# Kernel tuning notes

Measured on AMD Instinct MI355X. Metric: run time of the kernel, lower is better.

The kernel has to match this reference:

```python
import jax, jax.numpy as jnp
import numpy as np

N = 100000
EPS_BN = 1e-5


def setup_inputs() -> dict:
    key = jax.random.key(0)
    ks = jax.random.split(key, 12)
    x = jax.random.normal(ks[0], (N, 128), dtype=jnp.float32)
    edge_index = jax.random.randint(ks[1], (2, 800000), 0, N, dtype=jnp.int64)
    # GCNConv layer params (PyG: lin weight [out,in], bias added after aggregation)
    s = 1.0 / np.sqrt(128.0)
    W1 = jax.random.uniform(ks[2], (128, 128), jnp.float32, -s, s)
    b1 = jnp.zeros((128,), jnp.float32)
    W2 = jax.random.uniform(ks[3], (128, 128), jnp.float32, -s, s)
    b2 = jnp.zeros((128,), jnp.float32)
    # BatchNorm affine params
    g1 = jnp.ones((128,), jnp.float32)
    be1 = jnp.zeros((128,), jnp.float32)
    g2 = jnp.ones((128,), jnp.float32)
    be2 = jnp.zeros((128,), jnp.float32)
    # PReLU single shared parameter (torch init = 0.25)
    a = jnp.asarray(0.25, jnp.float32)
    return {"x": x, "edge_index": edge_index, "W1": W1, "b1": b1, "g1": g1,
            "be1": be1, "W2": W2, "b2": b2, "g2": g2, "be2": be2, "a": a}


def _gcn_conv(x, src, dst, deg_inv_sqrt, W, b):
    # x' = D^-1/2 (A+I) D^-1/2 (x W^T) + b  (self loops already in src/dst)
    h = x @ W.T                                   # [N, out]
    norm = deg_inv_sqrt[src] * deg_inv_sqrt[dst]  # [E+N]
    msg = h[src] * norm[:, None]                  # gather + scale
    out = jax.ops.segment_sum(msg, dst, num_segments=N)  # scatter-add
    return out + b


def _batchnorm(x, g, be):
    # training-mode BatchNorm1d over nodes (biased variance)
    mean = jnp.mean(x, axis=0)
    var = jnp.mean(jnp.square(x - mean), axis=0)
    return (x - mean) * jax.lax.rsqrt(var + EPS_BN) * g + be


def _prelu(x, a):
    return jnp.where(x > 0, x, a * x)


def reference(x, edge_index, W1, b1, g1, be1, W2, b2, g2, be2, a):
    # add self loops
    loops = jnp.arange(N, dtype=edge_index.dtype)
    src = jnp.concatenate([edge_index[0], loops])
    dst = jnp.concatenate([edge_index[1], loops])
    # symmetric normalization from in-degree at destinations
    deg = jax.ops.segment_sum(jnp.ones_like(dst, dtype=x.dtype), dst, num_segments=N)
    deg_inv_sqrt = jnp.where(deg > 0, jax.lax.rsqrt(deg), 0.0)

    h = _gcn_conv(x, src, dst, deg_inv_sqrt, W1, b1)
    h = _prelu(_batchnorm(h, g1, be1), a)
    h = _gcn_conv(h, src, dst, deg_inv_sqrt, W2, b2)
    h = _prelu(_batchnorm(h, g2, be2), a)
    return h
```

## Files before the change

### kernel.cpp

```cpp
#include <hip/hip_runtime.h>
#include <cstddef>
#include <cstdint>


#define EPS_BN 1e-5f
#define BN_BLOCKS 256

typedef short short8 __attribute__((ext_vector_type(8)));
typedef float f32x4 __attribute__((ext_vector_type(4)));

static __device__ __forceinline__ unsigned short f2b(float f) {
    union { float f; uint32_t u; } v; v.f = f;
    uint32_t u = v.u;
    return (unsigned short)((u + 0x7FFFu + ((u >> 16) & 1u)) >> 16);
}
static __device__ __forceinline__ float b2f(unsigned short h) {
    union { uint32_t u; float f; } v; v.u = ((uint32_t)h) << 16;
    return v.f;
}
static __device__ __forceinline__ float b2f_s(short h) { return b2f((unsigned short)h); }

__global__ __launch_bounds__(256) void k_count(const int* __restrict__ dst, int* __restrict__ cnt, int E) {
    int e = blockIdx.x * 256 + threadIdx.x;
    if (e < E) atomicAdd(&cnt[dst[e]], 1);
}

__global__ __launch_bounds__(256) void k_scanA(const int* __restrict__ cnt, int* __restrict__ partial, int n) {
    __shared__ int sd[256];
    int tid = threadIdx.x;
    int base = blockIdx.x * 1024 + tid * 4;
    int s = 0;
#pragma unroll
    for (int j = 0; j < 4; j++) { int idx = base + j; if (idx < n) s += cnt[idx]; }
    sd[tid] = s; __syncthreads();
    for (int off = 128; off > 0; off >>= 1) {
        if (tid < off) sd[tid] += sd[tid + off];
        __syncthreads();
    }
    if (tid == 0) partial[blockIdx.x] = sd[0];
}

__global__ __launch_bounds__(128) void k_scanB(int* partial, int nb) {
    __shared__ int sd[128];
    int t = threadIdx.x;
    sd[t] = (t < nb) ? partial[t] : 0;
    __syncthreads();
    for (int off = 1; off < 128; off <<= 1) {
        int v = (t >= off) ? sd[t - off] : 0;
        __syncthreads();
        sd[t] += v;
        __syncthreads();
    }
    if (t < nb) partial[t] = (t == 0) ? 0 : sd[t - 1];
}

__global__ __launch_bounds__(256) void k_scanC(const int* __restrict__ cnt, const int* __restrict__ partial,
                                               int* __restrict__ rowptr, float* __restrict__ dis, int n) {
    __shared__ int sd[256];
    int tid = threadIdx.x;
    int base = blockIdx.x * 1024 + tid * 4;
    int v[4]; int s = 0;
#pragma unroll
    for (int j = 0; j < 4; j++) { int idx = base + j; v[j] = (idx < n) ? cnt[idx] : 0; s += v[j]; }
    sd[tid] = s; __syncthreads();
    for (int off = 1; off < 256; off <<= 1) {
        int u = (tid >= off) ? sd[tid - off] : 0;
        __syncthreads();
        sd[tid] += u;
        __syncthreads();
    }
    int excl = partial[blockIdx.x] + ((tid == 0) ? 0 : sd[tid - 1]);
#pragma unroll
    for (int j = 0; j < 4; j++) {
        int idx = base + j;
        if (idx < n) {
            rowptr[idx] = excl;
            dis[idx] = rsqrtf((float)(v[j] + 1));
        }
        excl += v[j];
    }
}

__global__ __launch_bounds__(256) void k_fill(const int* __restrict__ src, const int* __restrict__ dst,
                                              const int* __restrict__ rowptr, int* __restrict__ fillc,
                                              int* __restrict__ colw, int E) {
    int e = blockIdx.x * 256 + threadIdx.x;
    if (e < E) {
        int d = dst[e];
        int pos = rowptr[d] + atomicAdd(&fillc[d], 1);
        colw[pos] = src[e];
    }
}

__global__ __launch_bounds__(256) void k_wprep(const float* __restrict__ W1, const float* __restrict__ W2,
                                               unsigned short* __restrict__ Wz1, unsigned short* __restrict__ Wz2) {
    int gi = blockIdx.x * 256 + threadIdx.x;
    const float* W = (gi < 16384) ? W1 : W2;
    unsigned short* Wz = (gi < 16384) ? Wz1 : Wz2;
    int idx = gi & 16383;
    int o = idx >> 7, k = idx & 127;
    int ct = o >> 4, nn = o & 15, ks = k >> 5, q = (k >> 3) & 3, j = k & 7;
    Wz[(ct * 4 + ks) * 512 + (q * 16 + nn) * 8 + j] = f2b(W[idx]);
}

__global__ __launch_bounds__(256) void k_gemm1(const float* __restrict__ X,
                                               const unsigned short* __restrict__ Wz,
                                               unsigned short* __restrict__ Yb, int n) {
    __shared__ unsigned short lds[16384];
    int tid = threadIdx.x;
    const short8* wsrc = (const short8*)Wz;
    short8* ldst = (short8*)lds;
#pragma unroll
    for (int i = 0; i < 8; i++) ldst[tid + 256 * i] = wsrc[tid + 256 * i];
    __syncthreads();

    int wave = tid >> 6, lane = tid & 63;
    int r0 = blockIdx.x * 64 + wave * 16;
    int mrow = lane & 15, quad = lane >> 4;
    int arow = r0 + mrow; if (arow > n - 1) arow = n - 1;
    const float* xr = X + (size_t)arow * 128;

    f32x4 acc[8];
#pragma unroll
    for (int ct = 0; ct < 8; ct++) acc[ct] = (f32x4){0.f, 0.f, 0.f, 0.f};

#pragma unroll
    for (int ks = 0; ks < 4; ks++) {
        int kb = ks * 32 + quad * 8;
        float4 x0 = *reinterpret_cast<const float4*>(xr + kb);
        float4 x1 = *reinterpret_cast<const float4*>(xr + kb + 4);
        short8 a;
        a[0] = (short)f2b(x0.x); a[1] = (short)f2b(x0.y); a[2] = (short)f2b(x0.z); a[3] = (short)f2b(x0.w);
        a[4] = (short)f2b(x1.x); a[5] = (short)f2b(x1.y); a[6] = (short)f2b(x1.z); a[7] = (short)f2b(x1.w);
#pragma unroll
        for (int ct = 0; ct < 8; ct++) {
            short8 b = *(const short8*)(lds + (ct * 4 + ks) * 512 + lane * 8);
            acc[ct] = __builtin_amdgcn_mfma_f32_16x16x32_bf16(a, b, acc[ct], 0, 0, 0);
        }
    }
#pragma unroll
    for (int i = 0; i < 4; i++) {
        int row = r0 + quad * 4 + i;
        if (row < n) {
#pragma unroll
            for (int ct = 0; ct < 8; ct++)
                Yb[(size_t)row * 128 + ct * 16 + mrow] = f2b(acc[ct][i]);
        }
    }
}

__global__ __launch_bounds__(256) void k_gemm2(const unsigned short* __restrict__ Ab,
                                               const unsigned short* __restrict__ Wz,
                                               const float* __restrict__ sc, const float* __restrict__ sh,
                                               const float* __restrict__ ap,
                                               unsigned short* __restrict__ Yb, int n) {
    __shared__ unsigned short lds[16384];
    int tid = threadIdx.x;
    const short8* wsrc = (const short8*)Wz;
    short8* ldst = (short8*)lds;
#pragma unroll
    for (int i = 0; i < 8; i++) ldst[tid + 256 * i] = wsrc[tid + 256 * i];
    __syncthreads();

    float alpha = ap[0];
    int wave = tid >> 6, lane = tid & 63;
    int r0 = blockIdx.x * 64 + wave * 16;
    int mrow = lane & 15, quad = lane >> 4;
    int arow = r0 + mrow; if (arow > n - 1) arow = n - 1;
    const unsigned short* ar = Ab + (size_t)arow * 128;

    f32x4 acc[8];
#pragma unroll
    for (int ct = 0; ct < 8; ct++) acc[ct] = (f32x4){0.f, 0.f, 0.f, 0.f};

#pragma unroll
    for (int ks = 0; ks < 4; ks++) {
        int kb = ks * 32 + quad * 8;
        short8 raw = *(const short8*)(ar + kb);
        float4 s0 = *reinterpret_cast<const float4*>(sc + kb);
        float4 s1 = *reinterpret_cast<const float4*>(sc + kb + 4);
        float4 t0 = *reinterpret_cast<const float4*>(sh + kb);
        float4 t1 = *reinterpret_cast<const float4*>(sh + kb + 4);
        float ss[8] = {s0.x, s0.y, s0.z, s0.w, s1.x, s1.y, s1.z, s1.w};
        float tt[8] = {t0.x, t0.y, t0.z, t0.w, t1.x, t1.y, t1.z, t1.w};
        short8 a;
#pragma unroll
        for (int j = 0; j < 8; j++) {
            float x = fmaf(b2f_s(raw[j]), ss[j], tt[j]);
            x = x > 0.f ? x : alpha * x;
            a[j] = (short)f2b(x);
        }
#pragma unroll
        for (int ct = 0; ct < 8; ct++) {
            short8 b = *(const short8*)(lds + (ct * 4 + ks) * 512 + lane * 8);
            acc[ct] = __builtin_amdgcn_mfma_f32_16x16x32_bf16(a, b, acc[ct], 0, 0, 0);
        }
    }
#pragma unroll
    for (int i = 0; i < 4; i++) {
        int row = r0 + quad * 4 + i;
        if (row < n) {
#pragma unroll
            for (int ct = 0; ct < 8; ct++)
                Yb[(size_t)row * 128 + ct * 16 + mrow] = f2b(acc[ct][i]);
        }
    }
}

__global__ __launch_bounds__(256) void k_agg(const unsigned short* __restrict__ Hb,
                                             const int* __restrict__ rowptr, const int* __restrict__ cnt,
                                             const int* __restrict__ colw, const float* __restrict__ dis,
                                             const float* __restrict__ bias,
                                             unsigned short* __restrict__ outb, int n) {
    int lane = threadIdx.x & 15;
    int node = blockIdx.x * 16 + (threadIdx.x >> 4);
    if (node >= n) return;
    int lo = lane * 8;
    float dn = dis[node];
    short8 hv = *(const short8*)(Hb + (size_t)node * 128 + lo);
    float acc[8];
#pragma unroll
    for (int j = 0; j < 8; j++) acc[j] = dn * b2f_s(hv[j]);
    int beg = rowptr[node];
    int num = cnt[node];
    const int* cw = colw + beg;
    int e = 0;
    for (; e + 4 <= num; e += 4) {
        int s0 = cw[e], s1 = cw[e + 1], s2 = cw[e + 2], s3 = cw[e + 3];
        float w0 = dis[s0], w1 = dis[s1], w2 = dis[s2], w3 = dis[s3];
        short8 n0 = *(const short8*)(Hb + (size_t)s0 * 128 + lo);
        short8 n1 = *(const short8*)(Hb + (size_t)s1 * 128 + lo);
        short8 n2 = *(const short8*)(Hb + (size_t)s2 * 128 + lo);
        short8 n3 = *(const short8*)(Hb + (size_t)s3 * 128 + lo);
#pragma unroll
        for (int j = 0; j < 8; j++) {
            acc[j] = fmaf(w0, b2f_s(n0[j]), acc[j]);
            acc[j] = fmaf(w1, b2f_s(n1[j]), acc[j]);
            acc[j] = fmaf(w2, b2f_s(n2[j]), acc[j]);
            acc[j] = fmaf(w3, b2f_s(n3[j]), acc[j]);
        }
    }
    for (; e < num; ++e) {
        int s = cw[e];
        float w = dis[s];
        short8 nb = *(const short8*)(Hb + (size_t)s * 128 + lo);
#pragma unroll
        for (int j = 0; j < 8; j++) acc[j] = fmaf(w, b2f_s(nb[j]), acc[j]);
    }
    const float4 bv0 = reinterpret_cast<const float4*>(bias)[lane * 2 + 0];
    const float4 bv1 = reinterpret_cast<const float4*>(bias)[lane * 2 + 1];
    float bb[8] = {bv0.x, bv0.y, bv0.z, bv0.w, bv1.x, bv1.y, bv1.z, bv1.w};
    short8 ov;
#pragma unroll
    for (int j = 0; j < 8; j++) ov[j] = (short)f2b(fmaf(dn, acc[j], bb[j]));
    *(short8*)(outb + (size_t)node * 128 + lo) = ov;
}

__global__ __launch_bounds__(256) void k_bnstats(const unsigned short* __restrict__ X, float* __restrict__ part, int n) {
    __shared__ float ls[16][128];
    __shared__ float lq[16][128];
    int tid = threadIdx.x;
    int rs = tid >> 4, g = tid & 15;
    float s[8], q[8];
#pragma unroll
    for (int j = 0; j < 8; j++) { s[j] = 0.f; q[j] = 0.f; }
#pragma unroll 4
    for (int r = blockIdx.x * 16 + rs; r < n; r += BN_BLOCKS * 16) {
        short8 v = *(const short8*)(X + (size_t)r * 128 + g * 8);
#pragma unroll
        for (int j = 0; j < 8; j++) {
            float f = b2f_s(v[j]);
            s[j] += f; q[j] = fmaf(f, f, q[j]);
        }
    }
#pragma unroll
    for (int j = 0; j < 8; j++) { ls[rs][g * 8 + j] = s[j]; lq[rs][g * 8 + j] = q[j]; }
    __syncthreads();
    for (int off = 8; off > 0; off >>= 1) {
        if (rs < off) {
#pragma unroll
            for (int j = 0; j < 8; j++) {
                ls[rs][g * 8 + j] += ls[rs + off][g * 8 + j];
                lq[rs][g * 8 + j] += lq[rs + off][g * 8 + j];
            }
        }
        __syncthreads();
    }
    if (tid < 128) part[blockIdx.x * 256 + tid] = ls[0][tid];
    else           part[blockIdx.x * 256 + tid] = lq[0][tid - 128];
}

__global__ __launch_bounds__(128) void k_bnparams(const float* __restrict__ part, const float* __restrict__ g,
                                                  const float* __restrict__ be, float* __restrict__ sc,
                                                  float* __restrict__ sh, float invN) {
    int f = threadIdx.x;
    float s = 0.f, q = 0.f;
#pragma unroll 8
    for (int b = 0; b < BN_BLOCKS; b++) {
        s += part[b * 256 + f];
        q += part[b * 256 + 128 + f];
    }
    float mean = s * invN;
    float var = q * invN - mean * mean;
    float rstd = rsqrtf(var + EPS_BN);
    float scale = g[f] * rstd;
    sc[f] = scale;
    sh[f] = fmaf(-mean, scale, be[f]);
}

__global__ __launch_bounds__(256) void k_bnact_f(const unsigned short* __restrict__ X, float* __restrict__ Y,
                                                 const float* __restrict__ sc, const float* __restrict__ sh,
                                                 const float* __restrict__ ap, int n8) {
    int i = blockIdx.x * 256 + threadIdx.x;
    if (i >= n8) return;
    float a = ap[0];
    int g = i & 15;
    const float4 s0 = reinterpret_cast<const float4*>(sc)[g * 2 + 0];
    const float4 s1 = reinterpret_cast<const float4*>(sc)[g * 2 + 1];
    const float4 t0 = reinterpret_cast<const float4*>(sh)[g * 2 + 0];
    const float4 t1 = reinterpret_cast<const float4*>(sh)[g * 2 + 1];
    float ss[8] = {s0.x, s0.y, s0.z, s0.w, s1.x, s1.y, s1.z, s1.w};
    float tt[8] = {t0.x, t0.y, t0.z, t0.w, t1.x, t1.y, t1.z, t1.w};
    short8 v = reinterpret_cast<const short8*>(X)[i];
    float out[8];
#pragma unroll
    for (int j = 0; j < 8; j++) {
        float x = fmaf(b2f_s(v[j]), ss[j], tt[j]);
        out[j] = x > 0.f ? x : a * x;
    }
    float4 o0 = {out[0], out[1], out[2], out[3]};
    float4 o1 = {out[4], out[5], out[6], out[7]};
    reinterpret_cast<float4*>(Y)[i * 2 + 0] = o0;
    reinterpret_cast<float4*>(Y)[i * 2 + 1] = o1;
}

extern "C" void kernel_launch(void* const* d_in, const int* in_sizes, int n_in,
                              void* d_out, int out_size, void* d_ws, size_t ws_size,
                              hipStream_t stream) {
    (void)n_in; (void)out_size; (void)ws_size;
    const float* x   = (const float*)d_in[0];
    const int*   ei  = (const int*)d_in[1];
    const float* W1  = (const float*)d_in[2];
    const float* b1  = (const float*)d_in[3];
    const float* g1  = (const float*)d_in[4];
    const float* be1 = (const float*)d_in[5];
    const float* W2  = (const float*)d_in[6];
    const float* b2  = (const float*)d_in[7];
    const float* g2  = (const float*)d_in[8];
    const float* be2 = (const float*)d_in[9];
    const float* ap  = (const float*)d_in[10];
    float* out = (float*)d_out;

    const int N = in_sizes[0] / 128;
    const int E = in_sizes[1] / 2;
    const int* srcIdx = ei;
    const int* dstIdx = ei + E;

    char* w = (char*)d_ws;
    size_t off = 0;
    auto alloc = [&](size_t bytes) { char* p = w + off; off += (bytes + 255) & ~(size_t)255; return p; };
    int*   cnt     = (int*)  alloc((size_t)N * 4);
    int*   fillc   = (int*)  alloc((size_t)N * 4);
    int*   rowptr  = (int*)  alloc((size_t)N * 4);
    int*   colw    = (int*)  alloc((size_t)E * 4);
    float* dis     = (float*)alloc((size_t)N * 4);
    int*   partial = (int*)  alloc(4096);
    float* part    = (float*)alloc((size_t)BN_BLOCKS * 256 * 4);
    float* sc1     = (float*)alloc(512);
    float* sh1     = (float*)alloc(512);
    float* sc2     = (float*)alloc(512);
    float* sh2     = (float*)alloc(512);
    unsigned short* Wz1 = (unsigned short*)alloc(16384 * 2);
    unsigned short* Wz2 = (unsigned short*)alloc(16384 * 2);
    unsigned short* bufH = (unsigned short*)alloc((size_t)N * 128 * 2);
    unsigned short* bufA = (unsigned short*)alloc((size_t)N * 128 * 2);

    const float invN = 1.0f / (float)N;
    const int NB = (N + 1023) / 1024;
    const int gE = (E + 255) / 256;
    const int n8 = N * 16;
    const int gGemm = (N + 63) / 64;
    const int gAgg  = (N + 15) / 16;

    hipMemsetAsync(cnt, 0, (size_t)N * 4, stream);
    hipMemsetAsync(fillc, 0, (size_t)N * 4, stream);

    k_wprep<<<128, 256, 0, stream>>>(W1, W2, Wz1, Wz2);

    k_count<<<gE, 256, 0, stream>>>(dstIdx, cnt, E);
    k_scanA<<<NB, 256, 0, stream>>>(cnt, partial, N);
    k_scanB<<<1, 128, 0, stream>>>(partial, NB);
    k_scanC<<<NB, 256, 0, stream>>>(cnt, partial, rowptr, dis, N);
    k_fill<<<gE, 256, 0, stream>>>(srcIdx, dstIdx, rowptr, fillc, colw, E);

    k_gemm1<<<gGemm, 256, 0, stream>>>(x, Wz1, bufH, N);
    k_agg<<<gAgg, 256, 0, stream>>>(bufH, rowptr, cnt, colw, dis, b1, bufA, N);
    k_bnstats<<<BN_BLOCKS, 256, 0, stream>>>(bufA, part, N);
    k_bnparams<<<1, 128, 0, stream>>>(part, g1, be1, sc1, sh1, invN);

    k_gemm2<<<gGemm, 256, 0, stream>>>(bufA, Wz2, sc1, sh1, ap, bufH, N);
    k_agg<<<gAgg, 256, 0, stream>>>(bufH, rowptr, cnt, colw, dis, b2, bufA, N);
    k_bnstats<<<BN_BLOCKS, 256, 0, stream>>>(bufA, part, N);
    k_bnparams<<<1, 128, 0, stream>>>(part, g2, be2, sc2, sh2, invN);
    k_bnact_f<<<(n8 + 255) / 256, 256, 0, stream>>>(bufA, out, sc2, sh2, ap, n8);
}
```

Measured before the change: 347.1 us.

## Partition CSR count/fill atomics by destination range and reuse rowptr as cursor

Count and fill kernels now use a fixed grid of 512 blocks split into 8 destination-range groups. Each group scans all edges but only does atomics for destinations in its range, which localises atomic traffic to one slice of the counters and is meant to improve cache and L2 locality. The fill step now does atomicAdd directly on rowptr, which turns it into an end pointer that aggregation corrects by subtracting cnt. This drops the separate fillc buffer and its memset. The cost is that the edge list is read 8 times in each of these kernels.

```diff
diff --git a/kernel.cpp b/kernel.cpp
--- a/kernel.cpp
+++ b/kernel.cpp
@@ -5,6 +5,7 @@
 
 #define EPS_BN 1e-5f
 #define BN_BLOCKS 256
+#define CSR_BLOCKS 512
 
 typedef short short8 __attribute__((ext_vector_type(8)));
 typedef float f32x4 __attribute__((ext_vector_type(4)));
@@ -20,9 +21,17 @@
 }
 static __device__ __forceinline__ float b2f_s(short h) { return b2f((unsigned short)h); }
 
-__global__ __launch_bounds__(256) void k_count(const int* __restrict__ dst, int* __restrict__ cnt, int E) {
-    int e = blockIdx.x * 256 + threadIdx.x;
-    if (e < E) atomicAdd(&cnt[dst[e]], 1);
+__global__ __launch_bounds__(256) void k_count(const int* __restrict__ dst, int* __restrict__ cnt,
+                                               int E, int N) {
+    int g = blockIdx.x & 7;
+    int sub = blockIdx.x >> 3;
+    int nsub = gridDim.x >> 3;
+    int lo = (int)((long)g * N / 8);
+    int hi = (int)((long)(g + 1) * N / 8);
+    for (int e = sub * 256 + threadIdx.x; e < E; e += nsub * 256) {
+        int d = dst[e];
+        if (d >= lo && d < hi) atomicAdd(&cnt[d], 1);
+    }
 }
 
 __global__ __launch_bounds__(256) void k_scanA(const int* __restrict__ cnt, int* __restrict__ partial, int n) {
@@ -82,13 +91,19 @@
 }
 
 __global__ __launch_bounds__(256) void k_fill(const int* __restrict__ src, const int* __restrict__ dst,
-                                              const int* __restrict__ rowptr, int* __restrict__ fillc,
-                                              int* __restrict__ colw, int E) {
-    int e = blockIdx.x * 256 + threadIdx.x;
-    if (e < E) {
+                                              int* __restrict__ rowptr, int* __restrict__ colw,
+                                              int E, int N) {
+    int g = blockIdx.x & 7;
+    int sub = blockIdx.x >> 3;
+    int nsub = gridDim.x >> 3;
+    int lo = (int)((long)g * N / 8);
+    int hi = (int)((long)(g + 1) * N / 8);
+    for (int e = sub * 256 + threadIdx.x; e < E; e += nsub * 256) {
         int d = dst[e];
-        int pos = rowptr[d] + atomicAdd(&fillc[d], 1);
-        colw[pos] = src[e];
+        if (d >= lo && d < hi) {
+            int pos = atomicAdd(&rowptr[d], 1);
+            colw[pos] = src[e];
+        }
     }
 }
 
@@ -221,8 +236,8 @@
     float acc[8];
 #pragma unroll
     for (int j = 0; j < 8; j++) acc[j] = dn * b2f_s(hv[j]);
-    int beg = rowptr[node];
     int num = cnt[node];
+    int beg = rowptr[node] - num;
     const int* cw = colw + beg;
     int e = 0;
     for (; e + 4 <= num; e += 4) {
@@ -360,7 +375,6 @@
     size_t off = 0;
     auto alloc = [&](size_t bytes) { char* p = w + off; off += (bytes + 255) & ~(size_t)255; return p; };
     int*   cnt     = (int*)  alloc((size_t)N * 4);
-    int*   fillc   = (int*)  alloc((size_t)N * 4);
     int*   rowptr  = (int*)  alloc((size_t)N * 4);
     int*   colw    = (int*)  alloc((size_t)E * 4);
     float* dis     = (float*)alloc((size_t)N * 4);
@@ -377,21 +391,19 @@
 
     const float invN = 1.0f / (float)N;
     const int NB = (N + 1023) / 1024;
-    const int gE = (E + 255) / 256;
     const int n8 = N * 16;
     const int gGemm = (N + 63) / 64;
     const int gAgg  = (N + 15) / 16;
 
     hipMemsetAsync(cnt, 0, (size_t)N * 4, stream);
-    hipMemsetAsync(fillc, 0, (size_t)N * 4, stream);
 
     k_wprep<<<128, 256, 0, stream>>>(W1, W2, Wz1, Wz2);
 
-    k_count<<<gE, 256, 0, stream>>>(dstIdx, cnt, E);
+    k_count<<<CSR_BLOCKS, 256, 0, stream>>>(dstIdx, cnt, E, N);
     k_scanA<<<NB, 256, 0, stream>>>(cnt, partial, N);
     k_scanB<<<1, 128, 0, stream>>>(partial, NB);
     k_scanC<<<NB, 256, 0, stream>>>(cnt, partial, rowptr, dis, N);
-    k_fill<<<gE, 256, 0, stream>>>(srcIdx, dstIdx, rowptr, fillc, colw, E);
+    k_fill<<<CSR_BLOCKS, 256, 0, stream>>>(srcIdx, dstIdx, rowptr, colw, E, N);
 
     k_gemm1<<<gGemm, 256, 0, stream>>>(x, Wz1, bufH, N);
     k_agg<<<gAgg, 256, 0, stream>>>(bufH, rowptr, cnt, colw, dis, b1, bufA, N);
```

Measured after the change: 347.3 us. About the same (+0.0%).
